# Optimization experiments

Measured on AMD Instinct MI355X. Metric: run time of the kernel, lower is better.

The kernel has to match this reference:

```python
import jax, jax.numpy as jnp
import numpy as np

D, H, KVH, HD = 2048, 16, 8, 128
D1, D2 = 32, 64  # get_decompose_dim(2048)
BITS = 8


def fake_quant(x, bits=BITS):
    # per-row (last-axis) symmetric fake quant with straight-through estimator
    qmax = float(2 ** (bits - 1) - 1)
    s = jnp.maximum(jnp.max(jnp.abs(x), axis=-1, keepdims=True) / qmax, 1e-8)
    q = jnp.clip(jnp.round(x / s), -qmax, qmax) * s
    return x + jax.lax.stop_gradient(q - x)


def rotate_half(x):
    h = x.shape[-1] // 2
    return jnp.concatenate([-x[..., h:], x[..., :h]], axis=-1)


def setup_inputs() -> dict:
    key = jax.random.key(0)
    ks = jax.random.split(key, 10)
    B, S = 1, 2048
    hidden_states = jax.random.normal(ks[0], (B, S, D), jnp.float32)
    # rotary embeddings
    inv_freq = 1.0 / (10000.0 ** (jnp.arange(0, HD, 2, dtype=jnp.float32) / HD))
    t = jnp.arange(S, dtype=jnp.float32)
    freqs = t[:, None] * inv_freq[None, :]
    emb = jnp.concatenate([freqs, freqs], axis=-1)
    cos, sin = jnp.cos(emb)[None], jnp.sin(emb)[None]  # [1,S,HD]
    # projection weights
    Wq = jax.random.normal(ks[1], (H * HD, D), jnp.float32) * 0.02
    Wk = jax.random.normal(ks[2], (KVH * HD, D), jnp.float32) * 0.02
    Wv = jax.random.normal(ks[3], (KVH * HD, D), jnp.float32) * 0.02
    Wo = jax.random.normal(ks[4], (D, H * HD), jnp.float32) * 0.02
    # learned invertible transforms (near-identity for conditioning)
    L = jnp.eye(D1) + 0.02 * jax.random.normal(ks[5], (D1, D1), jnp.float32)
    R = jnp.eye(D2) + 0.02 * jax.random.normal(ks[6], (D2, D2), jnp.float32)
    diag = 1.0 + 0.1 * jax.random.uniform(ks[7], (D,), jnp.float32)
    Tk = jnp.eye(HD) + 0.02 * jax.random.normal(ks[8], (HD, HD), jnp.float32)
    Tv = jnp.eye(HD) + 0.02 * jax.random.normal(ks[9], (HD, HD), jnp.float32)
    return dict(hidden_states=hidden_states, cos=cos, sin=sin, Wq=Wq, Wk=Wk,
                Wv=Wv, Wo=Wo, L=L, R=R, diag=diag, Tk=Tk, Tv=Tv)


def reference(hidden_states, cos, sin, Wq, Wk, Wv, Wo, L, R, diag, Tk, Tv):
    B, S, _ = hidden_states.shape
    groups = H // KVH
    scale = HD ** -0.5
    # ---- ln_trans: x' = (x * diag) @ kron(L, R) ----
    P = diag[:, None] * jnp.kron(L, R)               # [D, D]
    Pinv = jnp.kron(jnp.linalg.inv(L), jnp.linalg.inv(R)) * (1.0 / diag)[None, :]
    x = hidden_states @ P
    x_q = fake_quant(x)                               # per-token activation quant
    # ---- QKV with transform fused into weights (qa_trans), then weight quant ----
    q = x_q @ fake_quant(Wq @ Pinv.T).T               # [B,S,H*HD]
    k = x_q @ fake_quant(Wk @ Pinv.T).T               # [B,S,KVH*HD]
    Wv_eff = jnp.einsum('hd,khD->kdD', Tv, (Wv @ Pinv.T).reshape(KVH, HD, D))
    v = x_q @ fake_quant(Wv_eff.reshape(KVH * HD, D)).T  # v already in Tv space
    # ---- heads + RoPE ----
    q = q.reshape(B, S, H, HD).transpose(0, 2, 1, 3)
    k = k.reshape(B, S, KVH, HD).transpose(0, 2, 1, 3)
    v = v.reshape(B, S, KVH, HD).transpose(0, 2, 1, 3)
    c, s_ = cos[:, None], sin[:, None]                # [1,1,S,HD]
    q = q * c + rotate_half(q) * s_
    k = k * c + rotate_half(k) * s_
    # ---- kcache trans + quant: q @ inv(Tk)^T, k @ Tk (dot product preserved) ----
    q = q @ jnp.linalg.inv(Tk).T
    k = fake_quant(k @ Tk)
    v = fake_quant(v)
    # ---- eager causal attention with GQA ----
    k = jnp.repeat(k, groups, axis=1)
    v = jnp.repeat(v, groups, axis=1)
    scores = jnp.einsum('bhqd,bhkd->bhqk', q, k) * scale
    mask = jnp.tril(jnp.ones((S, S), bool))
    scores = jnp.where(mask, scores, jnp.finfo(scores.dtype).min)
    w = jax.nn.softmax(scores, axis=-1)
    o = jnp.einsum('bhqk,bhkd->bhqd', w, v)
    o = o.transpose(0, 2, 1, 3).reshape(B, S, H * HD)
    # ---- undo vcache trans per head, then quantized o_proj ----
    o = (o.reshape(B, S, H, HD) @ jnp.linalg.inv(Tv)).reshape(B, S, H * HD)
    out = fake_quant(o) @ fake_quant(Wo).T
    return out
```

## Files before the change

kernel.cpp:

```cpp
#include <hip/hip_runtime.h>
#include <math.h>

typedef unsigned short u16;
typedef __attribute__((ext_vector_type(8))) short bf16x8;
typedef __attribute__((ext_vector_type(4))) float f32x4;

__device__ __forceinline__ u16 f2bf(float x) {
    union { float f; unsigned int u; } c; c.f = x;
    unsigned int r = c.u + 0x7fffu + ((c.u >> 16) & 1u);
    return (u16)(r >> 16);
}
__device__ __forceinline__ float bf2f(u16 h) {
    union { unsigned int u; float f; } c; c.u = ((unsigned int)h) << 16;
    return c.f;
}
__device__ __forceinline__ bf16x8 ld16(const u16* p) {
    bf16x8 r;
    ((uint2*)&r)[0] = *(const uint2*)p;
    ((uint2*)&r)[1] = *(const uint2*)(p + 4);
    return r;
}
__device__ __forceinline__ void st8(u16* dst, uint4 r) {
    *(uint2*)dst = make_uint2(r.x, r.y);
    *(uint2*)(dst + 4) = make_uint2(r.z, r.w);
}

__global__ __launch_bounds__(1024) void gj4_kernel(
    const float* __restrict__ A0, float* __restrict__ I0,
    const float* __restrict__ A1, float* __restrict__ I1,
    const float* __restrict__ A2, float* __restrict__ I2,
    const float* __restrict__ A3, float* __restrict__ I3) {
    __shared__ float rowbuf[2][128];
    const float* A; float* out; int N;
    switch (blockIdx.x) {
        case 0:  A = A0; out = I0; N = 32;  break;
        case 1:  A = A1; out = I1; N = 64;  break;
        case 2:  A = A2; out = I2; N = 128; break;
        default: A = A3; out = I3; N = 128; break;
    }
    const int tid = threadIdx.x;
    const int i = tid >> 3, g = tid & 7, c0 = g * 16;
    const int rl = (i & 7) << 3;
    float r[16];
#pragma unroll
    for (int e = 0; e < 16; ++e) {
        int j = c0 + e;
        r[e] = (i < N && j < N) ? A[i * N + j] : ((i == j) ? 1.0f : 0.0f);
    }
    if (i == 0) {
        float ip = 1.0f / __shfl(r[0], rl, 64);
#pragma unroll
        for (int e = 0; e < 16; ++e)
            rowbuf[0][c0 + e] = (c0 + e == 0) ? ip : r[e] * ip;
    }
    __syncthreads();
    const int ng = N >> 4;
    for (int k16 = 0; k16 < ng; ++k16) {
#pragma unroll
        for (int e = 0; e < 16; ++e) {
            const int k = (k16 << 4) + e;
            const int pb = k & 1;
            float ci = __shfl(r[e], rl + k16, 64);
            float rb[16];
#pragma unroll
            for (int e2 = 0; e2 < 16; ++e2) rb[e2] = rowbuf[pb][c0 + e2];
            if (i == k) {
#pragma unroll
                for (int e2 = 0; e2 < 16; ++e2) r[e2] = rb[e2];
            } else {
#pragma unroll
                for (int e2 = 0; e2 < 16; ++e2) {
                    float v = (c0 + e2 == k) ? 0.0f : r[e2];
                    r[e2] = fmaf(-ci, rb[e2], v);
                }
            }
            if (k + 1 < N && i == k + 1) {
                const int en = (e + 1) & 15;
                const int gn = (e == 15) ? k16 + 1 : k16;
                float ip = 1.0f / __shfl(r[en], rl + gn, 64);
#pragma unroll
                for (int e2 = 0; e2 < 16; ++e2)
                    rowbuf[pb ^ 1][c0 + e2] = (c0 + e2 == k + 1) ? ip : r[e2] * ip;
            }
            __syncthreads();
        }
    }
    if (i < N)
#pragma unroll
        for (int e = 0; e < 16; ++e) {
            int j = c0 + e;
            if (j < N) out[i * N + j] = r[e];
        }
}

__global__ void rdiag_kernel(const float* __restrict__ d, float* __restrict__ rd) {
    int i = blockIdx.x * 256 + threadIdx.x;
    rd[i] = 1.0f / d[i];
}

template <int TA, int TB, int OUTQ>
__global__ __launch_bounds__(256) void kron_kernel(
    const float* __restrict__ X, const float* __restrict__ scIn,
    const float* __restrict__ A, const float* __restrict__ B,
    u16* __restrict__ Yq, float* __restrict__ Ysc, float* __restrict__ Yf) {
    __shared__ float Al[32 * 33];
    __shared__ float Bl[64 * 65];
    __shared__ float Xl[4][32 * 65];
    __shared__ float Tl[4][32 * 65];
    const int tid = threadIdx.x;
    for (int idx = tid; idx < 1024; idx += 256) {
        int c = idx >> 5, a = idx & 31;
        Al[c * 33 + a] = TA ? A[a * 32 + c] : A[c * 32 + a];
    }
    for (int idx = tid; idx < 4096; idx += 256) {
        int d = idx >> 6, b = idx & 63;
        Bl[d * 65 + b] = TB ? B[b * 64 + d] : B[d * 64 + b];
    }
    const int row0 = blockIdx.x * 4;
#pragma unroll
    for (int rr = 0; rr < 4; ++rr) {
        const float* xp = X + (size_t)(row0 + rr) * 2048;
        for (int j = tid; j < 2048; j += 256)
            Xl[rr][(j >> 6) * 65 + (j & 63)] = xp[j] * scIn[j];
    }
    __syncthreads();
    const int w = tid >> 6, lane = tid & 63;
    const int c = lane >> 1, b0 = (lane & 1) << 5;
    float t[32];
#pragma unroll
    for (int jj = 0; jj < 32; ++jj) t[jj] = 0.0f;
    for (int d = 0; d < 64; ++d) {
        float xv = Xl[w][c * 65 + d];
#pragma unroll
        for (int jj = 0; jj < 32; ++jj)
            t[jj] = fmaf(xv, Bl[d * 65 + b0 + jj], t[jj]);
    }
#pragma unroll
    for (int jj = 0; jj < 32; ++jj) Tl[w][c * 65 + b0 + jj] = t[jj];
    __syncthreads();
    const int a = lane >> 1, ob0 = (lane & 1) << 5;
    float y[32];
#pragma unroll
    for (int jj = 0; jj < 32; ++jj) y[jj] = 0.0f;
    for (int c2 = 0; c2 < 32; ++c2) {
        float av = Al[c2 * 33 + a];
#pragma unroll
        for (int jj = 0; jj < 32; ++jj)
            y[jj] = fmaf(av, Tl[w][c2 * 65 + ob0 + jj], y[jj]);
    }
    if (OUTQ) {
        float am = 0.0f;
#pragma unroll
        for (int jj = 0; jj < 32; ++jj) am = fmaxf(am, fabsf(y[jj]));
#pragma unroll
        for (int off = 1; off < 64; off <<= 1) am = fmaxf(am, __shfl_xor(am, off));
        float scale = fmaxf(am / 127.0f, 1e-8f);
        if (lane == 0) Ysc[row0 + w] = scale;
        u16* qp = Yq + (size_t)(row0 + w) * 2048 + lane * 32;
#pragma unroll
        for (int v4 = 0; v4 < 4; ++v4) {
            u16 qq[8];
#pragma unroll
            for (int e = 0; e < 8; ++e) {
                float v = rintf(y[v4 * 8 + e] / scale);
                v = fminf(fmaxf(v, -127.0f), 127.0f);
                qq[e] = f2bf(v);
            }
            uint4 pk;
            pk.x = qq[0] | ((unsigned)qq[1] << 16); pk.y = qq[2] | ((unsigned)qq[3] << 16);
            pk.z = qq[4] | ((unsigned)qq[5] << 16); pk.w = qq[6] | ((unsigned)qq[7] << 16);
            *(uint4*)(qp + v4 * 8) = pk;
        }
    } else {
        float* yp = Yf + (size_t)(row0 + w) * 2048 + lane * 32;
#pragma unroll
        for (int v4 = 0; v4 < 8; ++v4)
            *(float4*)(yp + v4 * 4) = make_float4(y[v4 * 4], y[v4 * 4 + 1],
                                                  y[v4 * 4 + 2], y[v4 * 4 + 3]);
    }
}

__global__ void split_s_kernel(const float* __restrict__ in, int ld, int cols,
                               u16* __restrict__ hi, u16* __restrict__ lo) {
    int idx = (blockIdx.x * 256 + threadIdx.x) * 4;
    int r = idx / cols, c = idx % cols;
    float4 v = *(const float4*)(in + (size_t)r * ld + c);
    ushort4 h, l;
    h.x = f2bf(v.x); l.x = f2bf(v.x - bf2f(h.x));
    h.y = f2bf(v.y); l.y = f2bf(v.y - bf2f(h.y));
    h.z = f2bf(v.z); l.z = f2bf(v.z - bf2f(h.z));
    h.w = f2bf(v.w); l.w = f2bf(v.w - bf2f(h.w));
    *(ushort4*)(hi + idx) = h;
    *(ushort4*)(lo + idx) = l;
}

__global__ void split_t_kernel(const float* __restrict__ in, u16* __restrict__ hi,
                               u16* __restrict__ lo, int rows, int cols) {
    __shared__ float t[32][33];
    int bx = blockIdx.x, by = blockIdx.y;
    int lx = threadIdx.x & 31, ly = threadIdx.x >> 5;
    for (int r = ly; r < 32; r += 8)
        t[r][lx] = in[(size_t)(by * 32 + r) * cols + bx * 32 + lx];
    __syncthreads();
    for (int r = ly; r < 32; r += 8) {
        float v = t[lx][r];
        size_t o = (size_t)(bx * 32 + r) * rows + by * 32 + lx;
        u16 h = f2bf(v);
        hi[o] = h;
        lo[o] = f2bf(v - bf2f(h));
    }
}

__global__ void trans16_kernel(const u16* __restrict__ in, u16* __restrict__ out,
                               int rows, int cols) {
    __shared__ u16 t[64][72];
    int bx = blockIdx.x, by = blockIdx.y;
    int tid = threadIdx.x;
#pragma unroll
    for (int it = 0; it < 2; ++it) {
        int ii = tid + it * 256;
        int r = ii >> 3, c8 = (ii & 7) * 8;
        uint4 v = *(const uint4*)(in + (size_t)(by * 64 + r) * cols + bx * 64 + c8);
        st8(&t[r][c8], v);
    }
    __syncthreads();
#pragma unroll
    for (int it = 0; it < 2; ++it) {
        int ii = tid + it * 256;
        int r = ii >> 3, c8 = (ii & 7) * 8;
        u16 tmp[8];
#pragma unroll
        for (int e = 0; e < 8; ++e) tmp[e] = t[c8 + e][r];
        uint4 v;
        v.x = tmp[0] | ((unsigned)tmp[1] << 16); v.y = tmp[2] | ((unsigned)tmp[3] << 16);
        v.z = tmp[4] | ((unsigned)tmp[5] << 16); v.w = tmp[6] | ((unsigned)tmp[7] << 16);
        *(uint4*)(out + (size_t)(bx * 64 + r) * rows + by * 64 + c8) = v;
    }
}

__global__ __launch_bounds__(256) void gemm_kernel(
    const u16* __restrict__ Ah, const u16* __restrict__ Al, int lda, long aZ, int aDiv,
    const u16* __restrict__ Bh, const u16* __restrict__ Bl, int ldb, long bZ, int bDiv,
    float* __restrict__ C, int ldc, long cZ, int cDiv, int K, float alpha) {
    const int m0 = blockIdx.y * 128, n0 = blockIdx.x * 128;
    const int z = blockIdx.z;
    {
        long ao = (long)(z >> aDiv) * aZ;
        long bo = (long)(z >> bDiv) * bZ;
        Ah += ao; Al += ao; Bh += bo; Bl += bo;
    }
    __shared__ u16 Ash[2][2][128][36];
    __shared__ u16 Bsh[2][2][128][36];

    const int tid = threadIdx.x, lane = tid & 63, wave = tid >> 6;
    const int wr = wave >> 1, wc = wave & 1;
    const int fr = lane & 15, fg8 = (lane >> 4) * 8;
    const int srow = tid >> 2, cc8 = (tid & 3) * 8;

    f32x4 acc[4][4];
#pragma unroll
    for (int m = 0; m < 4; ++m)
#pragma unroll
        for (int n = 0; n < 4; ++n) acc[m][n] = (f32x4)0.0f;

    uint4 rah0, rah1, ral0, ral1, rbh0, rbh1, rbl0, rbl1;
    const size_t aoff0 = (size_t)(m0 + srow) * lda + cc8;
    const size_t aoff1 = aoff0 + (size_t)64 * lda;
    const size_t boff0 = (size_t)(n0 + srow) * ldb + cc8;
    const size_t boff1 = boff0 + (size_t)64 * ldb;

#define G_LOAD(k0) { \
    rah0 = *(const uint4*)(Ah + aoff0 + (k0)); rah1 = *(const uint4*)(Ah + aoff1 + (k0)); \
    ral0 = *(const uint4*)(Al + aoff0 + (k0)); ral1 = *(const uint4*)(Al + aoff1 + (k0)); \
    rbh0 = *(const uint4*)(Bh + boff0 + (k0)); rbh1 = *(const uint4*)(Bh + boff1 + (k0)); \
    rbl0 = *(const uint4*)(Bl + boff0 + (k0)); rbl1 = *(const uint4*)(Bl + boff1 + (k0)); }
#define G_STORE(b) { \
    st8(&Ash[b][0][srow][cc8], rah0); st8(&Ash[b][0][srow + 64][cc8], rah1); \
    st8(&Ash[b][1][srow][cc8], ral0); st8(&Ash[b][1][srow + 64][cc8], ral1); \
    st8(&Bsh[b][0][srow][cc8], rbh0); st8(&Bsh[b][0][srow + 64][cc8], rbh1); \
    st8(&Bsh[b][1][srow][cc8], rbl0); st8(&Bsh[b][1][srow + 64][cc8], rbl1); }

    const int nk = K >> 5;
    G_LOAD(0);
    G_STORE(0);
    __syncthreads();
    int cur = 0;
    for (int ik = 0; ik < nk; ++ik) {
        if (ik + 1 < nk) G_LOAD((ik + 1) << 5);
        bf16x8 bh[4], bl[4];
#pragma unroll
        for (int n = 0; n < 4; ++n) {
            bh[n] = ld16(&Bsh[cur][0][wc * 64 + n * 16 + fr][fg8]);
            bl[n] = ld16(&Bsh[cur][1][wc * 64 + n * 16 + fr][fg8]);
        }
#pragma unroll
        for (int m = 0; m < 4; ++m) {
            bf16x8 ah = ld16(&Ash[cur][0][wr * 64 + m * 16 + fr][fg8]);
            bf16x8 al = ld16(&Ash[cur][1][wr * 64 + m * 16 + fr][fg8]);
#pragma unroll
            for (int n = 0; n < 4; ++n) {
                acc[m][n] = __builtin_amdgcn_mfma_f32_16x16x32_bf16(ah, bh[n], acc[m][n], 0, 0, 0);
                acc[m][n] = __builtin_amdgcn_mfma_f32_16x16x32_bf16(ah, bl[n], acc[m][n], 0, 0, 0);
                acc[m][n] = __builtin_amdgcn_mfma_f32_16x16x32_bf16(al, bh[n], acc[m][n], 0, 0, 0);
            }
        }
        if (ik + 1 < nk) G_STORE(cur ^ 1);
        __syncthreads();
        cur ^= 1;
    }
    const long co = (long)(z >> cDiv) * cZ;
#pragma unroll
    for (int m = 0; m < 4; ++m) {
        int row_b = m0 + wr * 64 + m * 16 + (fg8 >> 1);
#pragma unroll
        for (int n = 0; n < 4; ++n) {
            int col = n0 + wc * 64 + n * 16 + fr;
#pragma unroll
            for (int j = 0; j < 4; ++j)
                C[co + (long)(row_b + j) * ldc + col] = alpha * acc[m][n][j];
        }
    }
#undef G_LOAD
#undef G_STORE
}

__global__ __launch_bounds__(256) void gemm_int_kernel(
    const u16* __restrict__ A, int lda, const float* __restrict__ sa,
    const u16* __restrict__ B, int ldb, const float* __restrict__ sb,
    float* __restrict__ C, int ldc, int K) {
    const int m0 = blockIdx.y * 128, n0 = blockIdx.x * 128;
    __shared__ u16 Ash[2][128][36];
    __shared__ u16 Bsh[2][128][36];
    const int tid = threadIdx.x, lane = tid & 63, wave = tid >> 6;
    const int wr = wave >> 1, wc = wave & 1;
    const int fr = lane & 15, fg8 = (lane >> 4) * 8;
    const int srow = tid >> 2, cc8 = (tid & 3) * 8;
    f32x4 acc[4][4];
#pragma unroll
    for (int m = 0; m < 4; ++m)
#pragma unroll
        for (int n = 0; n < 4; ++n) acc[m][n] = (f32x4)0.0f;

    uint4 ra0, ra1, rb0, rb1;
    const size_t aoff0 = (size_t)(m0 + srow) * lda + cc8;
    const size_t aoff1 = aoff0 + (size_t)64 * lda;
    const size_t boff0 = (size_t)(n0 + srow) * ldb + cc8;
    const size_t boff1 = boff0 + (size_t)64 * ldb;
#define GI_LOAD(k0) { \
    ra0 = *(const uint4*)(A + aoff0 + (k0)); ra1 = *(const uint4*)(A + aoff1 + (k0)); \
    rb0 = *(const uint4*)(B + boff0 + (k0)); rb1 = *(const uint4*)(B + boff1 + (k0)); }
#define GI_STORE(b) { \
    st8(&Ash[b][srow][cc8], ra0); st8(&Ash[b][srow + 64][cc8], ra1); \
    st8(&Bsh[b][srow][cc8], rb0); st8(&Bsh[b][srow + 64][cc8], rb1); }
    const int nk = K >> 5;
    GI_LOAD(0);
    GI_STORE(0);
    __syncthreads();
    int cur = 0;
    for (int ik = 0; ik < nk; ++ik) {
        if (ik + 1 < nk) GI_LOAD((ik + 1) << 5);
        bf16x8 bfr[4];
#pragma unroll
        for (int n = 0; n < 4; ++n)
            bfr[n] = ld16(&Bsh[cur][wc * 64 + n * 16 + fr][fg8]);
#pragma unroll
        for (int m = 0; m < 4; ++m) {
            bf16x8 ah = ld16(&Ash[cur][wr * 64 + m * 16 + fr][fg8]);
#pragma unroll
            for (int n = 0; n < 4; ++n)
                acc[m][n] = __builtin_amdgcn_mfma_f32_16x16x32_bf16(ah, bfr[n], acc[m][n], 0, 0, 0);
        }
        if (ik + 1 < nk) GI_STORE(cur ^ 1);
        __syncthreads();
        cur ^= 1;
    }
#pragma unroll
    for (int m = 0; m < 4; ++m) {
        int row_b = m0 + wr * 64 + m * 16 + (fg8 >> 1);
#pragma unroll
        for (int n = 0; n < 4; ++n) {
            int col = n0 + wc * 64 + n * 16 + fr;
            float sc = sb[col];
#pragma unroll
            for (int j = 0; j < 4; ++j)
                C[(long)(row_b + j) * ldc + col] = acc[m][n][j] * sa[row_b + j] * sc;
        }
    }
#undef GI_LOAD
#undef GI_STORE
}

__global__ void rowquant_int_kernel(const float* __restrict__ x, u16* __restrict__ qi,
                                    float* __restrict__ sc, int cols) {
    __shared__ float red[256];
    int row = blockIdx.x, tid = threadIdx.x;
    const float* p = x + (size_t)row * cols;
    u16* q = qi + (size_t)row * cols;
    float m = 0.0f;
    for (int j = tid; j < cols; j += 256) m = fmaxf(m, fabsf(p[j]));
    red[tid] = m; __syncthreads();
    for (int s = 128; s > 0; s >>= 1) {
        if (tid < s) red[tid] = fmaxf(red[tid], red[tid + s]);
        __syncthreads();
    }
    float scale = fmaxf(red[0] / 127.0f, 1e-8f);
    if (tid == 0) sc[row] = scale;
    for (int j = tid; j < cols; j += 256) {
        float v = rintf(p[j] / scale);
        v = fminf(fmaxf(v, -127.0f), 127.0f);
        q[j] = f2bf(v);
    }
}

__global__ void rowquant_v_kernel(const float* __restrict__ x, int ld, int cb,
                                  u16* __restrict__ qi, float* __restrict__ sc) {
    int row = blockIdx.x;
    int lane = threadIdx.x & 63, w = threadIdx.x >> 6;
    if (w > 0) return;
    const float* p = x + (size_t)(row >> 3) * ld + cb + (row & 7) * 128;
    u16* q = qi + (size_t)row * 128;
    float2 v = *(const float2*)(p + lane * 2);
    float m = fmaxf(fabsf(v.x), fabsf(v.y));
#pragma unroll
    for (int off = 1; off < 64; off <<= 1) m = fmaxf(m, __shfl_xor(m, off));
    float scale = fmaxf(m / 127.0f, 1e-8f);
    if (lane == 0) sc[row] = scale;
    float a = rintf(v.x / scale), b = rintf(v.y / scale);
    a = fminf(fmaxf(a, -127.0f), 127.0f);
    b = fminf(fmaxf(b, -127.0f), 127.0f);
    unsigned pk = f2bf(a) | ((unsigned)f2bf(b) << 16);
    *(unsigned*)(q + lane * 2) = pk;
}

__global__ void rope_kernel(float* __restrict__ x, int ld, int cb,
                            const float* __restrict__ c, const float* __restrict__ s,
                            int nh) {
    int idx = blockIdx.x * 256 + threadIdx.x;
    int d = idx & 63;
    int t = idx >> 6;
    int h = t % nh;
    int sq = t / nh;
    size_t base = (size_t)sq * ld + cb + h * 128;
    float a = x[base + d], b = x[base + d + 64];
    float c1 = c[sq * 128 + d], s1 = s[sq * 128 + d];
    float c2 = c[sq * 128 + d + 64], s2 = s[sq * 128 + d + 64];
    x[base + d] = a * c1 - b * s1;
    x[base + d + 64] = b * c2 + a * s2;
}

__global__ __launch_bounds__(256, 2) void flash_kernel(
    const float* __restrict__ q2f,
    const u16* __restrict__ k2i, const float* __restrict__ ksc,
    const u16* __restrict__ vTi, const float* __restrict__ vsc,
    float* __restrict__ obuf, float* __restrict__ mlbuf) {
    const int h = blockIdx.x, part = blockIdx.y, qt = 31 - blockIdx.z, g = h >> 1;
    __shared__ u16 Ksh[2][64 * 128];
    __shared__ u16 Vsh[2][128 * 64];
    __shared__ u16 Psh[4][16 * 64];
    __shared__ float Kss[2][64];
    __shared__ float Vss[2][64];

    const int tid = threadIdx.x, lane = tid & 63, w = tid >> 6;
    const int lc = lane & 15, lg = lane >> 4;
    const float scale = 0.08838834764831845f;
    const float LOG2E = 1.4426950408889634f;
    const float THR = 10.0f;

    bf16x8 qh[4], ql[4];
    {
        int s = qt * 64 + w * 16 + lc;
        const float* qp = q2f + (size_t)s * 2048 + h * 128 + lg * 8;
#pragma unroll
        for (int kk = 0; kk < 4; ++kk) {
            float4 v0 = *(const float4*)(qp + kk * 32);
            float4 v1 = *(const float4*)(qp + kk * 32 + 4);
            float vv[8] = {v0.x, v0.y, v0.z, v0.w, v1.x, v1.y, v1.z, v1.w};
#pragma unroll
            for (int e = 0; e < 8; ++e) {
                float x = vv[e] * scale;
                u16 hh = f2bf(x);
                qh[kk][e] = (short)hh;
                ql[kk][e] = (short)f2bf(x - bf2f(hh));
            }
        }
    }

    f32x4 acc_o[8];
#pragma unroll
    for (int nn = 0; nn < 8; ++nn) acc_o[nn] = (f32x4)0.0f;
    float mj = -1e30f, lj = 0.0f;

    const int p0cnt = (qt + 2) >> 1;
    const int tn = (part == 0) ? p0cnt : (qt + 1 - p0cnt);
    const int t0 = (part == 0) ? 0 : p0cnt;

    const int kr = tid >> 2, kc = tid & 3;
    const int vd = tid >> 1, vc0 = (tid & 1) * 4;
    uint4 kg0, kg1, kg2, kg3, vg0, vg1, vg2, vg3;
    float sreg = 0.0f;

#define STAGE_LOAD(tg) { \
    const int j0_ = (tg) * 64; \
    const u16* kp_ = k2i + (size_t)(j0_ + kr) * 1024 + g * 128; \
    kg0 = *(const uint4*)(kp_ + kc * 8); \
    kg1 = *(const uint4*)(kp_ + (kc + 4) * 8); \
    kg2 = *(const uint4*)(kp_ + (kc + 8) * 8); \
    kg3 = *(const uint4*)(kp_ + (kc + 12) * 8); \
    const u16* vp_ = vTi + (size_t)(g * 128 + vd) * 2048 + j0_; \
    vg0 = *(const uint4*)(vp_ + vc0 * 8); \
    vg1 = *(const uint4*)(vp_ + (vc0 + 1) * 8); \
    vg2 = *(const uint4*)(vp_ + (vc0 + 2) * 8); \
    vg3 = *(const uint4*)(vp_ + (vc0 + 3) * 8); \
    if (tid < 64) sreg = ksc[(j0_ + tid) * 8 + g] * LOG2E; \
    else if (tid < 128) sreg = vsc[(j0_ + tid - 64) * 8 + g]; }

#define STAGE_WRITE(b) { \
    *(uint4*)(&Ksh[b][kr * 128 + ((kc ^ (kr & 7)) << 3)]) = kg0; \
    *(uint4*)(&Ksh[b][kr * 128 + (((kc + 4) ^ (kr & 7)) << 3)]) = kg1; \
    *(uint4*)(&Ksh[b][kr * 128 + (((kc + 8) ^ (kr & 7)) << 3)]) = kg2; \
    *(uint4*)(&Ksh[b][kr * 128 + (((kc + 12) ^ (kr & 7)) << 3)]) = kg3; \
    *(uint4*)(&Vsh[b][vd * 64 + ((vc0 ^ (vd & 7)) << 3)]) = vg0; \
    *(uint4*)(&Vsh[b][vd * 64 + (((vc0 + 1) ^ (vd & 7)) << 3)]) = vg1; \
    *(uint4*)(&Vsh[b][vd * 64 + (((vc0 + 2) ^ (vd & 7)) << 3)]) = vg2; \
    *(uint4*)(&Vsh[b][vd * 64 + (((vc0 + 3) ^ (vd & 7)) << 3)]) = vg3; \
    if (tid < 64) Kss[b][tid] = sreg; \
    else if (tid < 128) Vss[b][tid - 64] = sreg; }

    if (tn > 0) {
        STAGE_LOAD(t0);
        STAGE_WRITE(0);
    }
    __syncthreads();
    for (int t = 0; t < tn; ++t) {
        const int cur = t & 1;
        const int tg = t0 + t;
        if (t + 1 < tn) STAGE_LOAD(t0 + t + 1);

        f32x4 accs[4];
#pragma unroll
        for (int n = 0; n < 4; ++n) accs[n] = (f32x4)0.0f;
#pragma unroll
        for (int n = 0; n < 4; ++n) {
#pragma unroll
            for (int kk = 0; kk < 4; ++kk) {
                bf16x8 kf = ld16(&Ksh[cur][(n * 16 + lc) * 128 + (((kk * 4 + lg) ^ (lc & 7)) << 3)]);
                accs[n] = __builtin_amdgcn_mfma_f32_16x16x32_bf16(kf, qh[kk], accs[n], 0, 0, 0);
                accs[n] = __builtin_amdgcn_mfma_f32_16x16x32_bf16(kf, ql[kk], accs[n], 0, 0, 0);
            }
        }
#pragma unroll
        for (int n = 0; n < 4; ++n)
#pragma unroll
            for (int j = 0; j < 4; ++j)
                accs[n][j] *= Kss[cur][n * 16 + lg * 4 + j];
        if (tg == qt) {
            int qg = qt * 64 + w * 16 + lc;
#pragma unroll
            for (int n = 0; n < 4; ++n)
#pragma unroll
                for (int j = 0; j < 4; ++j) {
                    int kgl = tg * 64 + n * 16 + lg * 4 + j;
                    if (kgl > qg) accs[n][j] = -3.0e38f;
                }
        }

        float pm = accs[0][0];
#pragma unroll
        for (int n = 0; n < 4; ++n)
#pragma unroll
            for (int j = 0; j < 4; ++j) pm = fmaxf(pm, accs[n][j]);
        pm = fmaxf(pm, __shfl_xor(pm, 16));
        pm = fmaxf(pm, __shfl_xor(pm, 32));
        bool need = pm > mj + THR;
        float mn = need ? pm : mj;
        float sf = need ? exp2f(mj - mn) : 1.0f;
        mj = mn;
        if (__any(need)) {
            float sfj[4];
#pragma unroll
            for (int j = 0; j < 4; ++j) sfj[j] = __shfl(sf, lg * 4 + j);
#pragma unroll
            for (int nn = 0; nn < 8; ++nn)
#pragma unroll
                for (int j = 0; j < 4; ++j) acc_o[nn][j] *= sfj[j];
        }
        float rowsum = 0.0f;
#pragma unroll
        for (int n = 0; n < 4; ++n)
#pragma unroll
            for (int j = 0; j < 4; ++j) {
                float p = exp2f(accs[n][j] - mj);
                accs[n][j] = p;
                rowsum += p;
            }
        rowsum += __shfl_xor(rowsum, 16);
        rowsum += __shfl_xor(rowsum, 32);
        lj = lj * sf + rowsum;

#pragma unroll
        for (int n = 0; n < 4; ++n)
#pragma unroll
            for (int jp = 0; jp < 2; ++jp) {
                int k = n * 16 + lg * 4 + jp * 2;
                unsigned val = f2bf(accs[n][jp * 2] * Vss[cur][k]) |
                               ((unsigned)f2bf(accs[n][jp * 2 + 1] * Vss[cur][k + 1]) << 16);
                int cch = k >> 3;
                *(unsigned*)(&Psh[w][lc * 64 + ((cch ^ (lc & 7)) << 3) + (k & 7)]) = val;
            }
        bf16x8 pf[2];
#pragma unroll
        for (int kk = 0; kk < 2; ++kk)
            pf[kk] = ld16(&Psh[w][lc * 64 + (((kk * 4 + lg) ^ (lc & 7)) << 3)]);

#pragma unroll
        for (int nn = 0; nn < 8; ++nn) {
            int d = nn * 16 + lc;
#pragma unroll
            for (int kk = 0; kk < 2; ++kk) {
                bf16x8 vf = ld16(&Vsh[cur][d * 64 + (((kk * 4 + lg) ^ (d & 7)) << 3)]);
                acc_o[nn] = __builtin_amdgcn_mfma_f32_16x16x32_bf16(pf[kk], vf, acc_o[nn], 0, 0, 0);
            }
        }
        if (t + 1 < tn) STAGE_WRITE(cur ^ 1);
        __syncthreads();
    }
#undef STAGE_LOAD
#undef STAGE_WRITE

    float* op = obuf + (size_t)part * 4194304 + ((size_t)h * 2048 + qt * 64 + w * 16) * 128;
#pragma unroll
    for (int nn = 0; nn < 8; ++nn)
#pragma unroll
        for (int j = 0; j < 4; ++j)
            op[(lg * 4 + j) * 128 + nn * 16 + lc] = acc_o[nn][j];
    if (lg == 0) {
        int rs = h * 2048 + qt * 64 + w * 16 + lc;
        mlbuf[part * 65536 + rs] = mj;
        mlbuf[part * 65536 + 32768 + rs] = lj;
    }
}

__global__ void combine_split_kernel(const float* __restrict__ o01,
                                     const float* __restrict__ ml,
                                     u16* __restrict__ oh, u16* __restrict__ ol) {
    int idx = blockIdx.x * 256 + threadIdx.x;
    int hs = idx >> 7;
    float m0 = ml[hs], l0 = ml[32768 + hs];
    float m1 = ml[65536 + hs], l1 = ml[98304 + hs];
    float m = fmaxf(m0, m1);
    float w0 = exp2f(m0 - m), w1 = exp2f(m1 - m);
    float l = l0 * w0 + l1 * w1;
    float v = (o01[idx] * w0 + o01[4194304 + idx] * w1) / l;
    u16 h = f2bf(v);
    oh[idx] = h;
    ol[idx] = f2bf(v - bf2f(h));
}

__global__ void add2_kernel(const float* __restrict__ a, const float* __restrict__ b,
                            float* __restrict__ o) {
    int i = (blockIdx.x * 256 + threadIdx.x) * 4;
    float4 x = *(const float4*)(a + i);
    float4 y = *(const float4*)(b + i);
    x.x += y.x; x.y += y.y; x.z += y.z; x.w += y.w;
    *(float4*)(o + i) = x;
}

extern "C" void kernel_launch(void* const* d_in, const int* in_sizes, int n_in,
                              void* d_out, int out_size, void* d_ws, size_t ws_size,
                              hipStream_t stream) {
    const float* hidden = (const float*)d_in[0];
    const float* cosp   = (const float*)d_in[1];
    const float* sinp   = (const float*)d_in[2];
    const float* Wq     = (const float*)d_in[3];
    const float* Wk     = (const float*)d_in[4];
    const float* Wv     = (const float*)d_in[5];
    const float* Wo     = (const float*)d_in[6];
    const float* Lp     = (const float*)d_in[7];
    const float* Rp     = (const float*)d_in[8];
    const float* diag   = (const float*)d_in[9];
    const float* Tkp    = (const float*)d_in[10];
    const float* Tvp    = (const float*)d_in[11];
    float* out = (float*)d_out;

    const size_t MiB = 1ull << 20;
    char* W = (char*)d_ws;
    auto F = [&](size_t mb) { return (float*)(W + mb * MiB); };
    auto U = [&](size_t mb) { return (u16*)(W + mb * MiB); };
    const long HP2 = 2097152;

    float* dsc   = (float*)d_out;
    float* invL  = dsc;
    float* invR  = dsc + 1024;
    float* invTk = dsc + 5120;
    float* invTv = dsc + 21504;
    u16* sm = (u16*)(dsc + 37888);
    u16* invTk_sh = sm;              u16* invTk_sl = sm + 16384;
    u16* TkT_sh   = sm + 2 * 16384;  u16* TkT_sl   = sm + 3 * 16384;
    u16* invTvT_sh= sm + 4 * 16384;  u16* invTvT_sl= sm + 5 * 16384;
    u16* TvT_sh   = sm + 6 * 16384;  u16* TvT_sl   = sm + 7 * 16384;

    auto gemm = [&](dim3 grid,
                    const u16* Ah, const u16* Al, int lda, long aZ, int aDiv,
                    const u16* Bh, const u16* Bl, int ldb, long bZ, int bDiv,
                    float* C, int ldc, long cZ, int cDiv, int K, float alpha) {
        gemm_kernel<<<grid, 256, 0, stream>>>(Ah, Al, lda, aZ, aDiv,
            Bh, Bl, ldb, bZ, bDiv, C, ldc, cZ, cDiv, K, alpha);
    };

    float* xs    = F(88);
    float* wqkvs = xs + 2048;
    float* wqs   = wqkvs;
    float* wks   = wqkvs + 2048;
    float* wvs   = wqkvs + 3072;
    float* k2s   = wqkvs + 4096;
    float* vs    = k2s + 16384;
    float* o2s   = vs + 16384;
    float* wos   = o2s + 2048;
    float* rdiag = wos + 2048;

    gj4_kernel<<<4, 1024, 0, stream>>>(Lp, invL, Rp, invR, Tkp, invTk, Tvp, invTv);
    rdiag_kernel<<<8, 256, 0, stream>>>(diag, rdiag);
    split_s_kernel<<<16, 256, 0, stream>>>(invTk, 128, 128, invTk_sh, invTk_sl);
    split_t_kernel<<<dim3(4, 4), 256, 0, stream>>>(Tkp, TkT_sh, TkT_sl, 128, 128);
    split_t_kernel<<<dim3(4, 4), 256, 0, stream>>>(invTv, invTvT_sh, invTvT_sl, 128, 128);
    split_t_kernel<<<dim3(4, 4), 256, 0, stream>>>(Tvp, TvT_sh, TvT_sl, 128, 128);

    u16* Xi    = U(0);
    u16* WQKVi = U(8);
    u16* WVi   = U(20);
    float* WvP = F(24);
    kron_kernel<0, 0, 1><<<512, 256, 0, stream>>>(hidden, diag, Lp, Rp, Xi, xs, 0);
    kron_kernel<1, 1, 1><<<512, 256, 0, stream>>>(Wq, rdiag, invL, invR, WQKVi, wqs, 0);
    kron_kernel<1, 1, 1><<<256, 256, 0, stream>>>(Wk, rdiag, invL, invR, U(16), wks, 0);
    kron_kernel<1, 1, 0><<<256, 256, 0, stream>>>(Wv, rdiag, invL, invR, 0, 0, WvP);

    u16* WVPt_s = U(32);
    split_t_kernel<<<dim3(64, 32), 256, 0, stream>>>(WvP, WVPt_s, WVPt_s + HP2, 1024, 2048);
    float* WVf = F(72);
    gemm(dim3(16, 1, 8), TvT_sh, TvT_sl, 128, 0, 0,
         WVPt_s, WVPt_s + HP2, 1024, 128, 0, WVf, 2048, (long)128 * 2048, 0, 128, 1.0f);
    rowquant_int_kernel<<<1024, 256, 0, stream>>>(WVf, WVi, wvs, 2048);

    float* QKVf = F(40);
    gemm_int_kernel<<<dim3(32, 16), 256, 0, stream>>>(Xi, 2048, xs, WQKVi, 2048, wqkvs,
                                                      QKVf, 4096, 2048);

    rope_kernel<<<8192, 256, 0, stream>>>(QKVf, 4096, 0, cosp, sinp, 16);
    rope_kernel<<<4096, 256, 0, stream>>>(QKVf, 4096, 2048, cosp, sinp, 8);

    u16* KB_s = U(24);
    split_s_kernel<<<2048, 256, 0, stream>>>(QKVf + 2048, 4096, 1024, KB_s, KB_s + HP2);
    float* k2f = F(32);
    gemm(dim3(1, 16, 8), KB_s, KB_s + HP2, 1024, 128, 0,
         TkT_sh, TkT_sl, 128, 0, 0, k2f, 1024, 128, 0, 128, 1.0f);
    u16* k2i = U(8);
    rowquant_int_kernel<<<16384, 256, 0, stream>>>(k2f, k2i, k2s, 128);

    u16* Vi = U(12);
    rowquant_v_kernel<<<16384, 64, 0, stream>>>(QKVf, 4096, 3072, Vi, vs);
    u16* vTi = U(16);
    trans16_kernel<<<dim3(16, 32), 256, 0, stream>>>(Vi, vTi, 2048, 1024);

    u16* Q_s = U(24);
    split_s_kernel<<<4096, 256, 0, stream>>>(QKVf, 4096, 2048, Q_s, Q_s + 4194304);
    float* q2f = F(72);
    gemm(dim3(1, 16, 16), Q_s, Q_s + 4194304, 2048, 128, 0,
         invTk_sh, invTk_sl, 128, 0, 0, q2f, 2048, 128, 0, 128, 1.0f);

    float* o01 = F(40);
    float* ml  = F(32);
    flash_kernel<<<dim3(16, 2, 32), 256, 0, stream>>>(q2f, k2i, k2s, vTi, vs, o01, ml);
    u16* o_s = U(0);
    combine_split_kernel<<<16384, 256, 0, stream>>>(o01, ml, o_s, o_s + 4194304);

    float* o2f = F(16);
    gemm(dim3(1, 16, 16), o_s, o_s + 4194304, 128, 262144, 0,
         invTvT_sh, invTvT_sl, 128, 0, 0, o2f, 2048, 128, 0, 128, 1.0f);
    u16* o2i = U(32);
    rowquant_int_kernel<<<2048, 256, 0, stream>>>(o2f, o2i, o2s, 2048);
    u16* Woi = U(40);
    rowquant_int_kernel<<<2048, 256, 0, stream>>>(Wo, Woi, wos, 2048);
    float* C0 = F(48);
    float* C1 = F(64);
    gemm_int_kernel<<<dim3(16, 16), 256, 0, stream>>>(o2i, 2048, o2s, Woi, 2048, wos,
                                                      C0, 2048, 1024);
    gemm_int_kernel<<<dim3(16, 16), 256, 0, stream>>>(o2i + 1024, 2048, o2s, Woi + 1024,
                                                      2048, wos, C1, 2048, 1024);
    add2_kernel<<<4096, 256, 0, stream>>>(C0, C1, out);

    (void)in_sizes; (void)n_in; (void)out_size; (void)ws_size;
}
```

Baseline: 544.2 us.

## Process one row per block in kron kernel with 8 outputs per thread

New measurement: 523.5 us. 1.04x faster.

```diff
diff --git a/kernel.cpp b/kernel.cpp
--- a/kernel.cpp
+++ b/kernel.cpp
@@ -105,8 +105,9 @@
     u16* __restrict__ Yq, float* __restrict__ Ysc, float* __restrict__ Yf) {
     __shared__ float Al[32 * 33];
     __shared__ float Bl[64 * 65];
-    __shared__ float Xl[4][32 * 65];
-    __shared__ float Tl[4][32 * 65];
+    __shared__ float Xl[32 * 65];
+    __shared__ float Tl[32 * 65];
+    __shared__ float red[256];
     const int tid = threadIdx.x;
     for (int idx = tid; idx < 1024; idx += 256) {
         int c = idx >> 5, a = idx & 31;
@@ -116,67 +117,64 @@
         int d = idx >> 6, b = idx & 63;
         Bl[d * 65 + b] = TB ? B[b * 64 + d] : B[d * 64 + b];
     }
-    const int row0 = blockIdx.x * 4;
-#pragma unroll
-    for (int rr = 0; rr < 4; ++rr) {
-        const float* xp = X + (size_t)(row0 + rr) * 2048;
-        for (int j = tid; j < 2048; j += 256)
-            Xl[rr][(j >> 6) * 65 + (j & 63)] = xp[j] * scIn[j];
-    }
+    const int row = blockIdx.x;
+    const float* xp = X + (size_t)row * 2048;
+    for (int j = tid; j < 2048; j += 256)
+        Xl[(j >> 6) * 65 + (j & 63)] = xp[j] * scIn[j];
     __syncthreads();
-    const int w = tid >> 6, lane = tid & 63;
-    const int c = lane >> 1, b0 = (lane & 1) << 5;
-    float t[32];
-#pragma unroll
-    for (int jj = 0; jj < 32; ++jj) t[jj] = 0.0f;
+
+    const int c = tid >> 3, b0 = (tid & 7) * 8;
+    float t[8];
+#pragma unroll
+    for (int jj = 0; jj < 8; ++jj) t[jj] = 0.0f;
     for (int d = 0; d < 64; ++d) {
-        float xv = Xl[w][c * 65 + d];
-#pragma unroll
-        for (int jj = 0; jj < 32; ++jj)
+        float xv = Xl[c * 65 + d];
+#pragma unroll
+        for (int jj = 0; jj < 8; ++jj)
             t[jj] = fmaf(xv, Bl[d * 65 + b0 + jj], t[jj]);
     }
 #pragma unroll
-    for (int jj = 0; jj < 32; ++jj) Tl[w][c * 65 + b0 + jj] = t[jj];
+    for (int jj = 0; jj < 8; ++jj) Tl[c * 65 + b0 + jj] = t[jj];
     __syncthreads();
-    const int a = lane >> 1, ob0 = (lane & 1) << 5;
-    float y[32];
-#pragma unroll
-    for (int jj = 0; jj < 32; ++jj) y[jj] = 0.0f;
+
+    const int a = tid >> 3;
+    float y[8];
+#pragma unroll
+    for (int jj = 0; jj < 8; ++jj) y[jj] = 0.0f;
     for (int c2 = 0; c2 < 32; ++c2) {
         float av = Al[c2 * 33 + a];
 #pragma unroll
-        for (int jj = 0; jj < 32; ++jj)
-            y[jj] = fmaf(av, Tl[w][c2 * 65 + ob0 + jj], y[jj]);
-    }
+        for (int jj = 0; jj < 8; ++jj)
+            y[jj] = fmaf(av, Tl[c2 * 65 + b0 + jj], y[jj]);
+    }
+
     if (OUTQ) {
         float am = 0.0f;
 #pragma unroll
-        for (int jj = 0; jj < 32; ++jj) am = fmaxf(am, fabsf(y[jj]));
-#pragma unroll
-        for (int off = 1; off < 64; off <<= 1) am = fmaxf(am, __shfl_xor(am, off));
-        float scale = fmaxf(am / 127.0f, 1e-8f);
-        if (lane == 0) Ysc[row0 + w] = scale;
-        u16* qp = Yq + (size_t)(row0 + w) * 2048 + lane * 32;
-#pragma unroll
-        for (int v4 = 0; v4 < 4; ++v4) {
-            u16 qq[8];
-#pragma unroll
-            for (int e = 0; e < 8; ++e) {
-                float v = rintf(y[v4 * 8 + e] / scale);
-                v = fminf(fmaxf(v, -127.0f), 127.0f);
-                qq[e] = f2bf(v);
-            }
-            uint4 pk;
-            pk.x = qq[0] | ((unsigned)qq[1] << 16); pk.y = qq[2] | ((unsigned)qq[3] << 16);
-            pk.z = qq[4] | ((unsigned)qq[5] << 16); pk.w = qq[6] | ((unsigned)qq[7] << 16);
-            *(uint4*)(qp + v4 * 8) = pk;
-        }
+        for (int jj = 0; jj < 8; ++jj) am = fmaxf(am, fabsf(y[jj]));
+        red[tid] = am;
+        __syncthreads();
+        for (int s = 128; s > 0; s >>= 1) {
+            if (tid < s) red[tid] = fmaxf(red[tid], red[tid + s]);
+            __syncthreads();
+        }
+        float scale = fmaxf(red[0] / 127.0f, 1e-8f);
+        if (tid == 0) Ysc[row] = scale;
+        u16 qq[8];
+#pragma unroll
+        for (int e = 0; e < 8; ++e) {
+            float v = rintf(y[e] / scale);
+            v = fminf(fmaxf(v, -127.0f), 127.0f);
+            qq[e] = f2bf(v);
+        }
+        uint4 pk;
+        pk.x = qq[0] | ((unsigned)qq[1] << 16); pk.y = qq[2] | ((unsigned)qq[3] << 16);
+        pk.z = qq[4] | ((unsigned)qq[5] << 16); pk.w = qq[6] | ((unsigned)qq[7] << 16);
+        *(uint4*)(Yq + (size_t)row * 2048 + tid * 8) = pk;
     } else {
-        float* yp = Yf + (size_t)(row0 + w) * 2048 + lane * 32;
-#pragma unroll
-        for (int v4 = 0; v4 < 8; ++v4)
-            *(float4*)(yp + v4 * 4) = make_float4(y[v4 * 4], y[v4 * 4 + 1],
-                                                  y[v4 * 4 + 2], y[v4 * 4 + 3]);
+        float* yp = Yf + (size_t)row * 2048 + tid * 8;
+        *(float4*)yp = make_float4(y[0], y[1], y[2], y[3]);
+        *(float4*)(yp + 4) = make_float4(y[4], y[5], y[6], y[7]);
     }
 }
 
@@ -729,10 +727,10 @@
     u16* WQKVi = U(8);
     u16* WVi   = U(20);
     float* WvP = F(24);
-    kron_kernel<0, 0, 1><<<512, 256, 0, stream>>>(hidden, diag, Lp, Rp, Xi, xs, 0);
-    kron_kernel<1, 1, 1><<<512, 256, 0, stream>>>(Wq, rdiag, invL, invR, WQKVi, wqs, 0);
-    kron_kernel<1, 1, 1><<<256, 256, 0, stream>>>(Wk, rdiag, invL, invR, U(16), wks, 0);
-    kron_kernel<1, 1, 0><<<256, 256, 0, stream>>>(Wv, rdiag, invL, invR, 0, 0, WvP);
+    kron_kernel<0, 0, 1><<<2048, 256, 0, stream>>>(hidden, diag, Lp, Rp, Xi, xs, 0);
+    kron_kernel<1, 1, 1><<<2048, 256, 0, stream>>>(Wq, rdiag, invL, invR, WQKVi, wqs, 0);
+    kron_kernel<1, 1, 1><<<1024, 256, 0, stream>>>(Wk, rdiag, invL, invR, U(16), wks, 0);
+    kron_kernel<1, 1, 0><<<1024, 256, 0, stream>>>(Wv, rdiag, invL, invR, 0, 0, WvP);
 
     u16* WVPt_s = U(32);
     split_t_kernel<<<dim3(64, 32), 256, 0, stream>>>(WvP, WVPt_s, WVPt_s + HP2, 1024, 2048);
```
